# Kernel tuning notes

Measured on AMD Instinct MI355X. Metric: run time of the kernel, lower is better.

## Reference

```python
import jax, jax.numpy as jnp
import numpy as np

B, N, D = 2048, 128, 32   # samples, features, per-feature embed dim
H = 8                     # num_head
ND = N * D                # flattened width = 4096
U = D * N // H            # per-head units = 512
DH = D // H               # per-head output feature dim = 4


def setup_inputs() -> dict:
    key = jax.random.key(0)
    k_x, k_q, k_k, k_v, k_o = jax.random.split(key, 5)
    scale_w = 0.02  # keep QK^T logits in a sane range for softmax
    x = jax.random.normal(k_x, (B, N, D), dtype=jnp.float32)
    Wq = jax.random.normal(k_q, (H, ND, U), dtype=jnp.float32) * scale_w
    Wk = jax.random.normal(k_k, (H, ND, U), dtype=jnp.float32) * scale_w
    Wv = jax.random.normal(k_v, (H, ND, U), dtype=jnp.float32) * scale_w
    Wo = jax.random.normal(k_o, (D, D), dtype=jnp.float32) * (1.0 / np.sqrt(D))
    return {"x": x, "Wq": Wq, "Wk": Wk, "Wv": Wv, "Wo": Wo}


def reference(x, Wq, Wk, Wv, Wo):
    b, n, d = x.shape
    scale = d ** (-0.5)          # note: original scales by feature dim d, not head dim
    xf = x.reshape(b, n * d)     # (b, nd); the leading 1 axis in TF is vacuous
    # Batched per-head projections (collapses the Python head loop into one GEMM each)
    q = jnp.einsum('bf,hfu->hbu', xf, Wq)   # (H, b, U)
    k = jnp.einsum('bf,hfu->hbu', xf, Wk)   # (H, b, U)
    v = jnp.einsum('bf,hfu->hbu', xf, Wv)   # (H, b, U)
    scores = jax.nn.softmax(jnp.einsum('hbu,hcu->hbc', q, k) * scale, axis=-1)  # (H, b, b)
    av = jnp.einsum('hbc,hcu->hbu', scores, v)              # (H, b, U)
    # per-head reshape (b, U) -> (b, n, d/H), then concat heads along last dim
    av = av.reshape(H, b, n, d // H)                         # (H, b, n, dh)
    concat = jnp.transpose(av, (1, 2, 0, 3)).reshape(b, n, d)  # (b, n, d)
    return concat @ Wo  # dropout rate is 0 -> identity
```

## Files before the change

kernel.cpp:

```cpp
#include <hip/hip_runtime.h>
#include <stdint.h>
#include <math.h>

typedef short    s16x8 __attribute__((ext_vector_type(8)));
typedef float    f32x4 __attribute__((ext_vector_type(4)));
typedef uint32_t u32x4 __attribute__((ext_vector_type(4)));
typedef unsigned short u16x4 __attribute__((ext_vector_type(4)));
typedef unsigned short u16x8 __attribute__((ext_vector_type(8)));

__device__ __forceinline__ uint16_t f2bf(float f) {
  union { float f; uint32_t u; } v; v.f = f;
  uint32_t r = v.u + 0x7fffu + ((v.u >> 16) & 1u);
  return (uint16_t)(r >> 16);
}
__device__ __forceinline__ float bf2f(uint16_t h) {
  union { uint32_t u; float f; } v; v.u = ((uint32_t)h) << 16;
  return v.f;
}

__device__ __forceinline__ void gld16(const void* g, void* l) {
  __builtin_amdgcn_global_load_lds(
      (const __attribute__((address_space(1))) void*)g,
      (__attribute__((address_space(3))) void*)l, 16, 0, 0);
}

__global__ __launch_bounds__(256) void cvt_x(const float* __restrict__ x,
                                             uint16_t* __restrict__ xf,
                                             float* __restrict__ rs) {
  if (blockIdx.x < 64) rs[blockIdx.x * 256 + threadIdx.x] = 0.f;
  size_t i = ((size_t)blockIdx.x * 256 + threadIdx.x) * 4;
  f32x4 v = *(const f32x4*)(x + i);
  u16x4 o = { f2bf(v.x), f2bf(v.y), f2bf(v.z), f2bf(v.w) };
  *(u16x4*)(xf + i) = o;
}

__global__ __launch_bounds__(256) void wtrans(const float* __restrict__ W0,
                                              const float* __restrict__ W1,
                                              const float* __restrict__ W2,
                                              uint16_t* __restrict__ Wt) {
  const int z = blockIdx.z;
  const float* W = (z < 8 ? W0 : (z < 16 ? W1 : W2)) + (size_t)(z & 7) * (4096 * 512);
  const int f0 = blockIdx.x * 64, u0 = blockIdx.y * 32;
  __shared__ float t[64][33];
  const int tid = threadIdx.x;
  {
    const int fi = tid >> 2, uu = (tid & 3) * 8;
    const float* src = W + (size_t)(f0 + fi) * 512 + u0 + uu;
    f32x4 v0 = *(const f32x4*)src;
    f32x4 v1 = *(const f32x4*)(src + 4);
    t[fi][uu] = v0.x; t[fi][uu + 1] = v0.y; t[fi][uu + 2] = v0.z; t[fi][uu + 3] = v0.w;
    t[fi][uu + 4] = v1.x; t[fi][uu + 5] = v1.y; t[fi][uu + 6] = v1.z; t[fi][uu + 7] = v1.w;
  }
  __syncthreads();
  {
    const int uo = tid >> 3, fo = (tid & 7) * 8;
    u16x8 o = { f2bf(t[fo][uo]),     f2bf(t[fo + 1][uo]), f2bf(t[fo + 2][uo]),
                f2bf(t[fo + 3][uo]), f2bf(t[fo + 4][uo]), f2bf(t[fo + 5][uo]),
                f2bf(t[fo + 6][uo]), f2bf(t[fo + 7][uo]) };
    *(u16x8*)&Wt[((size_t)z * 512 + u0 + uo) * 4096 + f0 + fo] = o;
  }
}

template <int MODE>
__global__ __launch_bounds__(512, 2) void gemm_bt(
    const uint16_t* __restrict__ A, size_t sAz,
    const uint16_t* __restrict__ B, size_t sBz,
    void* __restrict__ C0, void* __restrict__ C1,
    int K, float scale, float* __restrict__ rs) {
  const int tid = threadIdx.x;
  const int wave = tid >> 6, lane = tid & 63;
  const int quad = lane >> 4, l16 = lane & 15;
  const int wm = wave >> 2, wn = wave & 3;
  const int wnh = wn >> 1, wnl = wn & 1;
  const int m0 = blockIdx.y * 256, n0 = blockIdx.x * 256;
  int z = blockIdx.z, kh = 0, Kloop = K;
  if (MODE == 3) { kh = z >> 3; z &= 7; Kloop = K >> 1; }
  A += (size_t)z * sAz + (size_t)kh * Kloop;
  B += (size_t)z * sBz + (size_t)kh * Kloop;

  __shared__ __align__(16) uint16_t lds[65536];

  f32x4 acc[8][4];
#pragma unroll
  for (int i = 0; i < 8; i++)
#pragma unroll
    for (int j = 0; j < 4; j++) acc[i][j] = f32x4{0.f, 0.f, 0.f, 0.f};
  s16x8 af[4][2], bq0[2][2], bq1[2][2];

  const int lrow = lane >> 3;
  const int cs = ((lane & 7) ^ (lrow & 7)) * 8;
  const uint16_t* gA = A + (size_t)(m0 + wave * 8 + lrow) * K + cs;
  const uint16_t* gB = B + (size_t)(n0 + wave * 8 + lrow) * K + cs;
  const size_t rs64 = (size_t)64 * K;
  const int stW = wave * 512;

#define STAGE(buf, mat, half, t)                                               \
  do {                                                                         \
    const uint16_t* gsrc =                                                     \
        ((mat) ? gB : gA) + (size_t)(half) * 128 * K + (size_t)(t) * 64;       \
    uint16_t* sdst =                                                           \
        &lds[(buf) * 32768 + (mat) * 16384 + (half) * 8192 + stW];             \
    gld16(gsrc, sdst);                                                         \
    gld16(gsrc + rs64, sdst + 4096);                                           \
  } while (0)

#define LOAD_A(buf, ih)                                                        \
  do {                                                                         \
    const uint16_t* ba = &lds[(buf) * 32768 + wm * 8192];                      \
    _Pragma("unroll") for (int i_ = 0; i_ < 4; i_++)                           \
      _Pragma("unroll") for (int k_ = 0; k_ < 2; k_++)                         \
        af[i_][k_] = *(const s16x8*)&ba[((ih) * 64 + i_ * 16 + l16) * 64 +     \
                                        ((k_ * 4 + quad) ^ (l16 & 7)) * 8];    \
  } while (0)

#define LOAD_B(buf, jh, bq)                                                    \
  do {                                                                         \
    const uint16_t* bb = &lds[(buf) * 32768 + 16384 + wnh * 8192];             \
    _Pragma("unroll") for (int j_ = 0; j_ < 2; j_++)                           \
      _Pragma("unroll") for (int k_ = 0; k_ < 2; k_++)                         \
        bq[j_][k_] = *(const s16x8*)&bb[(wnl * 64 + (jh) * 32 + j_ * 16 + l16) \
                                            * 64 +                             \
                                        ((k_ * 4 + quad) ^ (l16 & 7)) * 8];    \
  } while (0)

#define MMQ(ih, jh, bq)                                                        \
  do {                                                                         \
    __builtin_amdgcn_s_setprio(1);                                             \
    _Pragma("unroll") for (int i_ = 0; i_ < 4; i_++)                           \
      _Pragma("unroll") for (int j_ = 0; j_ < 2; j_++)                         \
        _Pragma("unroll") for (int k_ = 0; k_ < 2; k_++)                       \
          acc[(ih) * 4 + i_][(jh) * 2 + j_] =                                  \
              __builtin_amdgcn_mfma_f32_16x16x32_bf16(                         \
                  af[i_][k_], bq[j_][k_],                                      \
                  acc[(ih) * 4 + i_][(jh) * 2 + j_], 0, 0, 0);                 \
    __builtin_amdgcn_s_setprio(0);                                             \
  } while (0)

#define BAR __builtin_amdgcn_s_barrier()
#define LGKM0 asm volatile("s_waitcnt lgkmcnt(0)" ::: "memory")
#define VMW(n) asm volatile("s_waitcnt vmcnt(" #n ")" ::: "memory")

  STAGE(0, 1, 0, 0); STAGE(0, 1, 1, 0);
  STAGE(0, 0, 0, 0); STAGE(0, 0, 1, 0);
  STAGE(1, 1, 0, 1); STAGE(1, 1, 1, 1);
  VMW(4); BAR;

  const int L = (Kloop >> 7) - 1;
  for (int it = 0; it < L; ++it) {
    const int t1 = 2 * it + 1, t2 = 2 * it + 2, t3 = 2 * it + 3;
    LOAD_A(0, 0); LOAD_B(0, 0, bq0); STAGE(1, 0, 0, t1);
    BAR; LGKM0; MMQ(0, 0, bq0); BAR;
    LOAD_B(0, 1, bq1); STAGE(1, 0, 1, t1);
    BAR; LGKM0; MMQ(0, 1, bq1); BAR;
    LOAD_A(0, 1); STAGE(0, 1, 0, t2);
    BAR; LGKM0; MMQ(1, 0, bq0); BAR;
    STAGE(0, 1, 1, t2);
    BAR; LGKM0; MMQ(1, 1, bq1); VMW(4); BAR;
    LOAD_A(1, 0); LOAD_B(1, 0, bq0); STAGE(0, 0, 0, t2);
    BAR; LGKM0; MMQ(0, 0, bq0); BAR;
    LOAD_B(1, 1, bq1); STAGE(0, 0, 1, t2);
    BAR; LGKM0; MMQ(0, 1, bq1); BAR;
    LOAD_A(1, 1); STAGE(1, 1, 0, t3);
    BAR; LGKM0; MMQ(1, 0, bq0); BAR;
    STAGE(1, 1, 1, t3);
    BAR; LGKM0; MMQ(1, 1, bq1); VMW(4); BAR;
  }
  {
    const int t1 = 2 * L + 1;
    LOAD_A(0, 0); LOAD_B(0, 0, bq0); STAGE(1, 0, 0, t1);
    BAR; LGKM0; MMQ(0, 0, bq0); BAR;
    LOAD_B(0, 1, bq1); STAGE(1, 0, 1, t1);
    BAR; LGKM0; MMQ(0, 1, bq1); BAR;
    LOAD_A(0, 1);
    BAR; LGKM0; MMQ(1, 0, bq0); BAR;
    MMQ(1, 1, bq1); VMW(0); BAR;
    LOAD_A(1, 0); LOAD_B(1, 0, bq0); LGKM0; MMQ(0, 0, bq0);
    LOAD_B(1, 1, bq1); LGKM0; MMQ(0, 1, bq1);
    LOAD_A(1, 1); LGKM0; MMQ(1, 0, bq0);
    MMQ(1, 1, bq1);
  }

  const int mb = m0 + wm * 128 + quad * 4;
  const int nb = n0 + wn * 64 + l16;
  if (MODE == 4) {
    if (z < 16) {
      uint16_t* C = (uint16_t*)C0 + ((size_t)z << 20);
#pragma unroll
      for (int i = 0; i < 8; i++)
#pragma unroll
        for (int j = 0; j < 4; j++)
#pragma unroll
          for (int r = 0; r < 4; r++)
            C[(size_t)(mb + i * 16 + r) * 512 + (nb + j * 16)] = f2bf(acc[i][j][r]);
    } else {
      uint16_t* C = (uint16_t*)C1 + ((size_t)(z - 16) << 20);
#pragma unroll
      for (int i = 0; i < 8; i++)
#pragma unroll
        for (int j = 0; j < 4; j++) {
          u16x4 o = { f2bf(acc[i][j][0]), f2bf(acc[i][j][1]),
                      f2bf(acc[i][j][2]), f2bf(acc[i][j][3]) };
          *(u16x4*)&C[(size_t)(nb + j * 16) * 2048 + (mb + i * 16)] = o;
        }
    }
  } else if (MODE == 2) {
    uint16_t* C = (uint16_t*)C0 + ((size_t)z << 22);
    float* rz = rs + (z << 11);
    float si[8][4];
#pragma unroll
    for (int i = 0; i < 8; i++)
#pragma unroll
      for (int r = 0; r < 4; r++) si[i][r] = 0.f;
#pragma unroll
    for (int i = 0; i < 8; i++)
#pragma unroll
      for (int j = 0; j < 4; j++)
#pragma unroll
        for (int r = 0; r < 4; r++) {
          float e = exp2f(fmaf(acc[i][j][r], scale, -43.2808512f));
          uint16_t hb = f2bf(e);
          C[(size_t)(mb + i * 16 + r) * 2048 + (nb + j * 16)] = hb;
          si[i][r] += bf2f(hb);
        }
#pragma unroll
    for (int i = 0; i < 8; i++)
#pragma unroll
      for (int r = 0; r < 4; r++) {
        float s = si[i][r];
        s += __shfl_xor(s, 1);
        s += __shfl_xor(s, 2);
        s += __shfl_xor(s, 4);
        s += __shfl_xor(s, 8);
        si[i][r] = s;
      }
    if (l16 == 0) {
#pragma unroll
      for (int i = 0; i < 8; i++)
#pragma unroll
        for (int r = 0; r < 4; r++)
          atomicAdd(&rz[mb + i * 16 + r], si[i][r]);
    }
  } else {
    float* C = (float*)(kh ? C1 : C0) + ((size_t)z << 20);
    const float* rz = rs + (z << 11);
#pragma unroll
    for (int i = 0; i < 8; i++)
#pragma unroll
      for (int r = 0; r < 4; r++) {
        float w = 1.0f / rz[mb + i * 16 + r];
#pragma unroll
        for (int j = 0; j < 4; j++)
          C[(size_t)(mb + i * 16 + r) * 512 + (nb + j * 16)] = acc[i][j][r] * w;
      }
  }
#undef STAGE
#undef LOAD_A
#undef LOAD_B
#undef MMQ
#undef BAR
#undef LGKM0
#undef VMW
}

__global__ __launch_bounds__(256) void out_proj(const float* __restrict__ av0,
                                                const float* __restrict__ av1,
                                                const float* __restrict__ Wo,
                                                float* __restrict__ out) {
  __shared__ float lw[1024];
  const int tid = threadIdx.x;
#pragma unroll
  for (int i = 0; i < 4; i++) lw[tid + i * 256] = Wo[tid + i * 256];
  __syncthreads();
  const int p = blockIdx.x * 256 + tid;
  const int b = p >> 7, n = p & 127;
  float c[32];
#pragma unroll
  for (int hh = 0; hh < 8; hh++) {
    size_t idx = ((size_t)hh * 2048 + b) * 512 + n * 4;
    f32x4 v = *(const f32x4*)(av0 + idx);
    f32x4 w = *(const f32x4*)(av1 + idx);
    c[hh * 4] = v.x + w.x; c[hh * 4 + 1] = v.y + w.y;
    c[hh * 4 + 2] = v.z + w.z; c[hh * 4 + 3] = v.w + w.w;
  }
  float o[32];
#pragma unroll
  for (int d = 0; d < 32; d++) o[d] = 0.f;
#pragma unroll
  for (int j = 0; j < 32; j++) {
    float cj = c[j];
#pragma unroll
    for (int d = 0; d < 32; d++) o[d] = fmaf(cj, lw[j * 32 + d], o[d]);
  }
  float* dst = out + (size_t)p * 32;
#pragma unroll
  for (int i = 0; i < 8; i++) {
    f32x4 v = { o[i * 4], o[i * 4 + 1], o[i * 4 + 2], o[i * 4 + 3] };
    *(f32x4*)(dst + i * 4) = v;
  }
}

extern "C" void kernel_launch(void* const* d_in, const int* in_sizes, int n_in,
                              void* d_out, int out_size, void* d_ws, size_t ws_size,
                              hipStream_t stream) {
  const float* x  = (const float*)d_in[0];
  const float* Wq = (const float*)d_in[1];
  const float* Wk = (const float*)d_in[2];
  const float* Wv = (const float*)d_in[3];
  const float* Wo = (const float*)d_in[4];
  float* out = (float*)d_out;

  uint8_t* ws = (uint8_t*)d_ws;
  uint16_t* Wt  = (uint16_t*)(ws);
  uint16_t* P   = (uint16_t*)(ws);
  float*    av0 = (float*)(ws + 67108864);
  uint16_t* xf  = (uint16_t*)(ws + 100663296);
  uint16_t* q   = (uint16_t*)(ws + 117440512);
  float*    av1 = (float*)(ws + 117440512);
  uint16_t* vt  = (uint16_t*)(ws + 150994944);
  float*    rs  = (float*)(ws + 167772160);

  const size_t WtH = (size_t)512 * 4096;
  const float scale2 = 0.17677669529663687f * 1.4426950408889634f;

  cvt_x<<<8192, 256, 0, stream>>>(x, xf, rs);
  wtrans<<<dim3(64, 16, 24), 256, 0, stream>>>(Wq, Wk, Wv, Wt);

  gemm_bt<4><<<dim3(2, 8, 24), 512, 0, stream>>>(
      xf, 0, Wt, WtH, q, vt, 4096, 0.f, nullptr);

  gemm_bt<2><<<dim3(8, 8, 8), 512, 0, stream>>>(
      q, (size_t)2048 * 512, q + (size_t)8 * 2048 * 512, (size_t)2048 * 512,
      P, nullptr, 512, scale2, rs);

  gemm_bt<3><<<dim3(2, 8, 16), 512, 0, stream>>>(
      P, (size_t)2048 * 2048, vt, (size_t)512 * 2048,
      av0, av1, 2048, 0.f, rs);

  out_proj<<<1024, 256, 0, stream>>>(av0, av1, Wo, out);
}
```

Baseline: 550.1 us.

## Use a smaller-tile 128x128 GEMM kernel for the QKV projection

Adds a new 256-thread GEMM kernel with 128x128 tiles, an XOR-swizzled LDS layout and a simple two-barrier load/compute loop, used only for the QKV projection. The old 256x256, 512-thread pipelined kernel is renamed and kept for the scores and attention-value GEMMs. The QKV launch goes from 384 blocks to 1536, which improves CU fill and occupancy. In exchange each block reuses less data and the new loop has no software pipelining, so global loads are not overlapped with MFMA work.

```diff
diff --git a/kernel.cpp b/kernel.cpp
--- a/kernel.cpp
+++ b/kernel.cpp
@@ -62,7 +62,94 @@
 }
 
 template <int MODE>
-__global__ __launch_bounds__(512, 2) void gemm_bt(
+__global__ __launch_bounds__(256, 4) void gemm_bt(
+    const uint16_t* __restrict__ A, size_t sAz,
+    const uint16_t* __restrict__ B, size_t sBz,
+    void* __restrict__ C0, void* __restrict__ C1,
+    int K, float scale, float* __restrict__ rs) {
+  const int tid = threadIdx.x;
+  const int wave = tid >> 6, lane = tid & 63;
+  const int quad = lane >> 4, l16 = lane & 15;
+  const int wrow = (wave >> 1) * 64, wcol = (wave & 1) * 64;
+  const int m0 = blockIdx.y * 128, n0 = blockIdx.x * 128;
+  int z = blockIdx.z, kh = 0, Kloop = K;
+  if (MODE == 3) { kh = z >> 3; z &= 7; Kloop = K >> 1; }
+  A += (size_t)z * sAz + (size_t)kh * Kloop;
+  B += (size_t)z * sBz + (size_t)kh * Kloop;
+
+  __shared__ __align__(16) uint16_t lA[128 * 64];
+  __shared__ __align__(16) uint16_t lB[128 * 64];
+
+  f32x4 acc[4][4];
+#pragma unroll
+  for (int i = 0; i < 4; i++)
+#pragma unroll
+    for (int j = 0; j < 4; j++) acc[i][j] = f32x4{0.f, 0.f, 0.f, 0.f};
+
+  const int lrow = lane >> 3;
+  const int cs = ((lane & 7) ^ (lrow & 7)) * 8;
+  const int rs0 = wave * 8;
+  const uint16_t* gA = A + (size_t)(m0 + rs0 + lrow) * K + cs;
+  const uint16_t* gB = B + (size_t)(n0 + rs0 + lrow) * K + cs;
+  const size_t row32 = (size_t)32 * K;
+  uint16_t* sA = &lA[rs0 * 64];
+  uint16_t* sB = &lB[rs0 * 64];
+
+  for (int k0 = 0; k0 < Kloop; k0 += 64) {
+    __syncthreads();
+#pragma unroll
+    for (int g = 0; g < 4; g++) {
+      gld16(gA + g * row32, sA + g * 2048);
+      gld16(gB + g * row32, sB + g * 2048);
+    }
+    gA += 64; gB += 64;
+    __syncthreads();
+#pragma unroll
+    for (int h = 0; h < 2; h++) {
+      s16x8 af[4], bfr[4];
+      const int fsw = (((h * 4 + quad) ^ (l16 & 7)) * 8);
+#pragma unroll
+      for (int i = 0; i < 4; i++)
+        af[i] = *(const s16x8*)&lA[(wrow + i * 16 + l16) * 64 + fsw];
+#pragma unroll
+      for (int j = 0; j < 4; j++)
+        bfr[j] = *(const s16x8*)&lB[(wcol + j * 16 + l16) * 64 + fsw];
+#pragma unroll
+      for (int i = 0; i < 4; i++)
+#pragma unroll
+        for (int j = 0; j < 4; j++)
+          acc[i][j] = __builtin_amdgcn_mfma_f32_16x16x32_bf16(af[i], bfr[j], acc[i][j], 0, 0, 0);
+    }
+  }
+
+  const int mb = m0 + wrow + quad * 4;
+  const int nb = n0 + wcol + l16;
+  if (MODE == 4) {
+    if (z < 16) {
+      uint16_t* C = (uint16_t*)C0 + ((size_t)z << 20);
+#pragma unroll
+      for (int i = 0; i < 4; i++)
+#pragma unroll
+        for (int j = 0; j < 4; j++)
+#pragma unroll
+          for (int r = 0; r < 4; r++)
+            C[(size_t)(mb + i * 16 + r) * 512 + (nb + j * 16)] = f2bf(acc[i][j][r]);
+    } else {
+      uint16_t* C = (uint16_t*)C1 + ((size_t)(z - 16) << 20);
+#pragma unroll
+      for (int i = 0; i < 4; i++)
+#pragma unroll
+        for (int j = 0; j < 4; j++) {
+          u16x4 o = { f2bf(acc[i][j][0]), f2bf(acc[i][j][1]),
+                      f2bf(acc[i][j][2]), f2bf(acc[i][j][3]) };
+          *(u16x4*)&C[(size_t)(nb + j * 16) * 2048 + (mb + i * 16)] = o;
+        }
+    }
+  }
+}
+
+template <int MODE>
+__global__ __launch_bounds__(512, 2) void gemm_bt8(
     const uint16_t* __restrict__ A, size_t sAz,
     const uint16_t* __restrict__ B, size_t sBz,
     void* __restrict__ C0, void* __restrict__ C1,
@@ -182,28 +269,7 @@
 
   const int mb = m0 + wm * 128 + quad * 4;
   const int nb = n0 + wn * 64 + l16;
-  if (MODE == 4) {
-    if (z < 16) {
-      uint16_t* C = (uint16_t*)C0 + ((size_t)z << 20);
-#pragma unroll
-      for (int i = 0; i < 8; i++)
-#pragma unroll
-        for (int j = 0; j < 4; j++)
-#pragma unroll
-          for (int r = 0; r < 4; r++)
-            C[(size_t)(mb + i * 16 + r) * 512 + (nb + j * 16)] = f2bf(acc[i][j][r]);
-    } else {
-      uint16_t* C = (uint16_t*)C1 + ((size_t)(z - 16) << 20);
-#pragma unroll
-      for (int i = 0; i < 8; i++)
-#pragma unroll
-        for (int j = 0; j < 4; j++) {
-          u16x4 o = { f2bf(acc[i][j][0]), f2bf(acc[i][j][1]),
-                      f2bf(acc[i][j][2]), f2bf(acc[i][j][3]) };
-          *(u16x4*)&C[(size_t)(nb + j * 16) * 2048 + (mb + i * 16)] = o;
-        }
-    }
-  } else if (MODE == 2) {
+  if (MODE == 2) {
     uint16_t* C = (uint16_t*)C0 + ((size_t)z << 22);
     float* rz = rs + (z << 11);
     float si[8][4];
@@ -325,14 +391,14 @@
   cvt_x<<<8192, 256, 0, stream>>>(x, xf, rs);
   wtrans<<<dim3(64, 16, 24), 256, 0, stream>>>(Wq, Wk, Wv, Wt);
 
-  gemm_bt<4><<<dim3(2, 8, 24), 512, 0, stream>>>(
+  gemm_bt<4><<<dim3(4, 16, 24), 256, 0, stream>>>(
       xf, 0, Wt, WtH, q, vt, 4096, 0.f, nullptr);
 
-  gemm_bt<2><<<dim3(8, 8, 8), 512, 0, stream>>>(
+  gemm_bt8<2><<<dim3(8, 8, 8), 512, 0, stream>>>(
       q, (size_t)2048 * 512, q + (size_t)8 * 2048 * 512, (size_t)2048 * 512,
       P, nullptr, 512, scale2, rs);
 
-  gemm_bt<3><<<dim3(2, 8, 16), 512, 0, stream>>>(
+  gemm_bt8<3><<<dim3(2, 8, 16), 512, 0, stream>>>(
       P, (size_t)2048 * 2048, vt, (size_t)512 * 2048,
       av0, av1, 2048, 0.f, rs);
 
```

New measurement: 564.6 us. +2.6%, slower.
